# Performance work log

Measured on AMD Instinct MI355X. Metric: run time of the kernel, lower is better.

## Reference

```python
import jax, jax.numpy as jnp
import numpy as np

NU, NI, D, H, E, NQ = 200000, 100000, 64, 64, 1000000, 100000


def setup_inputs() -> dict:
    key = jax.random.key(0)
    ks = jax.random.split(key, 16)
    s = 0.05
    inp = {
        'user_emb': jax.random.normal(ks[0], (NU, D), jnp.float32) * s,
        'item_emb': jax.random.normal(ks[1], (NI, D), jnp.float32) * s,
        'W1': jax.random.normal(ks[2], (6, D, H), jnp.float32) * s,
        'b1': jnp.zeros((6, H), jnp.float32),
        'W2': jax.random.normal(ks[3], (6, H, H), jnp.float32) * s,
        'b2': jnp.zeros((6, H), jnp.float32),
        'dec_w1': jax.random.normal(ks[4], (2 * H, H), jnp.float32) * s,
        'dec_b1': jnp.zeros((H,), jnp.float32),
        'dec_w2': jax.random.normal(ks[5], (H, 4), jnp.float32) * s,
        'dec_b2': jnp.zeros((4,), jnp.float32),
    }
    for name, k in [('edge_view', ks[6]), ('edge_save', ks[7]), ('edge_buy', ks[8])]:
        src = jax.random.randint(k, (E,), 0, NU, jnp.int64 if jax.config.jax_enable_x64 else jnp.int32)
        dst = jax.random.randint(jax.random.fold_in(k, 1), (E,), 0, NI, src.dtype)
        inp[name] = jnp.stack([src, dst])  # [2, E], row0=user, row1=item
    inp['user_ids'] = jax.random.randint(ks[9], (NQ,), 0, NU, jnp.int32)
    inp['item_ids'] = jax.random.randint(ks[10], (NQ,), 0, NI, jnp.int32)
    return inp


def _gcn_conv(h_src, src, dst, n_src, n_dst, W, b):
    # GCNConv (add_self_loops=False) on a bipartite relation:
    # out[d] = sum_e 1/sqrt(deg_src[src_e]) * 1/sqrt(deg_dst[d]) * (x W)[src_e] + b
    h = h_src @ W  # [n_src, H]
    ones = jnp.ones(src.shape[0], h.dtype)
    deg_s = jax.ops.segment_sum(ones, src, num_segments=n_src)
    deg_d = jax.ops.segment_sum(ones, dst, num_segments=n_dst)
    inv_s = jnp.where(deg_s > 0, jax.lax.rsqrt(jnp.maximum(deg_s, 1.0)), 0.0)
    inv_d = jnp.where(deg_d > 0, jax.lax.rsqrt(jnp.maximum(deg_d, 1.0)), 0.0)
    norm = inv_s[src] * inv_d[dst]  # [E]
    msg = h[src] * norm[:, None]    # [E, H]  (dominant memory traffic)
    return jax.ops.segment_sum(msg, dst, num_segments=n_dst) + b


def _hetero_layer(xu, xi, edges, W, b, aggr):
    # relations 0..2: user->item (view,save,buy); 3..5: item->user (reverses)
    item_outs = jnp.stack([_gcn_conv(xu, e[0], e[1], NU, NI, W[k], b[k])
                           for k, e in enumerate(edges)])
    user_outs = jnp.stack([_gcn_conv(xi, e[1], e[0], NI, NU, W[k + 3], b[k + 3])
                           for k, e in enumerate(edges)])
    if aggr == 'max':
        return user_outs.max(0), item_outs.max(0)
    return user_outs.sum(0), item_outs.sum(0)


def reference(user_emb, item_emb, W1, b1, W2, b2, dec_w1, dec_b1, dec_w2, dec_b2,
              edge_view, edge_save, edge_buy, user_ids, item_ids):
    edges = [edge_view, edge_save, edge_buy]
    xu, xi = _hetero_layer(user_emb, item_emb, edges, W1, b1, 'max')
    xu, xi = jax.nn.relu(xu), jax.nn.relu(xi)
    xu, xi = _hetero_layer(xu, xi, edges, W2, b2, 'sum')
    edge_emb = jnp.concatenate([xu[user_ids], xi[item_ids]], axis=-1)  # [NQ, 2H]
    h = jax.nn.relu(edge_emb @ dec_w1 + dec_b1)  # dropout in eval mode = identity
    return h @ dec_w2 + dec_b2  # [NQ, 4]
```

## Files before the change

### kernel.cpp

```cpp
#include <hip/hip_runtime.h>
#include <hip/hip_fp16.h>
#include <math.h>

#define NUV 200000
#define NIV 100000
#define EV  1000000
#define NQV 100000
#define NC  (3 * NIV + 3 * NUV)
#define EV6 (6 * EV)

struct alignas(8) H4 { __half2 a, b; };

__global__ __launch_bounds__(256) void k_tohalf(const float* __restrict__ inu,
                                                const float* __restrict__ ini,
                                                __half* __restrict__ outu,
                                                __half* __restrict__ outi) {
    const int NU4 = NUV * 16;
    const int NTOT = NU4 + NIV * 16;
    int i = blockIdx.x * 256 + threadIdx.x;
    if (i < NTOT) {
        const float* in = (i < NU4) ? inu : ini;
        __half* out = (i < NU4) ? outu : outi;
        int j = (i < NU4) ? i : (i - NU4);
        float4 v = ((const float4*)in)[j];
        H4 o;
        o.a = __floats2half2_rn(v.x, v.y);
        o.b = __floats2half2_rn(v.z, v.w);
        ((H4*)out)[j] = o;
    }
}

__global__ __launch_bounds__(256) void k_count(const int* __restrict__ e0,
                                               const int* __restrict__ e1,
                                               const int* __restrict__ e2,
                                               int* __restrict__ cnt,
                                               int* __restrict__ rk_i,
                                               int* __restrict__ rk_u) {
    int k = blockIdx.y;
    const int* ed = (k == 0) ? e0 : (k == 1) ? e1 : e2;
    int e = blockIdx.x * 256 + threadIdx.x;
    if (e < EV) {
        int u = ed[e], i = ed[EV + e];
        rk_i[(size_t)k * EV + e] = atomicAdd(&cnt[k * NIV + i], 1);
        rk_u[(size_t)k * EV + e] = atomicAdd(&cnt[3 * NIV + k * NUV + u], 1);
    }
}

__global__ __launch_bounds__(256) void k_scan1(const int* __restrict__ cnt,
                                               int* __restrict__ S,
                                               int* __restrict__ bsum,
                                               float* __restrict__ invs) {
    __shared__ int tmp[256];
    int idx = blockIdx.x * 256 + threadIdx.x;
    int v = (idx < NC) ? cnt[idx] : 0;
    if (idx < NC) invs[idx] = (v > 0) ? (1.0f / sqrtf((float)v)) : 0.0f;
    tmp[threadIdx.x] = v;
    __syncthreads();
    for (int off = 1; off < 256; off <<= 1) {
        int t = (threadIdx.x >= off) ? tmp[threadIdx.x - off] : 0;
        __syncthreads();
        tmp[threadIdx.x] += t;
        __syncthreads();
    }
    if (idx < NC) S[idx] = tmp[threadIdx.x] - v;
    if (threadIdx.x == 255) bsum[blockIdx.x] = tmp[255];
}

__global__ __launch_bounds__(64) void k_scan2(int* __restrict__ bsum, int nb) {
    int lane = threadIdx.x;
    int carry = 0;
    for (int base = 0; base < nb; base += 64) {
        int i = base + lane;
        int v = (i < nb) ? bsum[i] : 0;
        int orig = v;
        #pragma unroll
        for (int off = 1; off < 64; off <<= 1) {
            int t = __shfl_up(v, off, 64);
            if (lane >= off) v += t;
        }
        if (i < nb) bsum[i] = carry + v - orig;
        carry += __shfl(v, 63, 64);
    }
}

__global__ __launch_bounds__(256) void k_scan3(int* __restrict__ S,
                                               const int* __restrict__ bsum) {
    int idx = blockIdx.x * 256 + threadIdx.x;
    if (idx < NC) S[idx] += bsum[blockIdx.x];
    if (idx == 0) S[NC] = EV6;
}

__global__ __launch_bounds__(256) void k_fill(const int* __restrict__ e0,
                                              const int* __restrict__ e1,
                                              const int* __restrict__ e2,
                                              const float* __restrict__ invs,
                                              const int* __restrict__ S,
                                              const int* __restrict__ rk_i,
                                              const int* __restrict__ rk_u,
                                              float2* __restrict__ ent) {
    int k = blockIdx.y;
    const int* ed = (k == 0) ? e0 : (k == 1) ? e1 : e2;
    int e = blockIdx.x * 256 + threadIdx.x;
    if (e < EV) {
        int u = ed[e], i = ed[EV + e];
        float nm = invs[k * NIV + i] * invs[3 * NIV + k * NUV + u];
        int p1 = S[k * NIV + i] + rk_i[(size_t)k * EV + e];
        ent[p1] = make_float2(__int_as_float(u), nm);
        int p2 = S[3 * NIV + k * NUV + u] + rk_u[(size_t)k * EV + e];
        ent[p2] = make_float2(__int_as_float(i), nm);
    }
}

template <int MODE, bool HOUT>
__global__ __launch_bounds__(256, 4) void k_agg(const __half* __restrict__ x_i,
                                                const __half* __restrict__ x_u,
                                                const float2* __restrict__ ent,
                                                const int* __restrict__ S,
                                                const float* __restrict__ Wall,
                                                const float* __restrict__ ball,
                                                void* __restrict__ out_i,
                                                void* __restrict__ out_u) {
    __shared__ float sAcc[3][16][68];
    __shared__ int nextT;

    const int NWG = NIV / 16 + NUV / 16;
    const int q = NWG / 8, r = NWG % 8;
    int xcd = blockIdx.x % 8, pos = blockIdx.x / 8;
    int wg = (xcd < r) ? (xcd * (q + 1) + pos) : (r * (q + 1) + (xcd - r) * q + pos);

    const int nb_i = NIV / 16;
    bool item_side = wg < nb_i;
    const __half* x = item_side ? x_i : x_u;
    const float* Wb = item_side ? Wall : Wall + 3 * 4096;
    const float* bb = item_side ? ball : ball + 192;
    void* outp      = item_side ? out_i : out_u;
    int n_dst       = item_side ? NIV : NUV;
    int seg_base    = item_side ? 0 : 3 * NIV;
    int d0          = (item_side ? wg : (wg - nb_i)) * 16;

    if (threadIdx.x == 0) nextT = 32;
    __syncthreads();

    int sgid = threadIdx.x >> 3;
    int ls   = threadIdx.x & 7;
    int lane = threadIdx.x & 63;

    int task = sgid;
    while (task < 48) {
        int rel = task >> 4, node = task & 15;
        int idx = seg_base + rel * n_dst + d0 + node;
        int st = S[idx], en = S[idx + 1];

        float4 a0 = make_float4(0.f, 0.f, 0.f, 0.f);
        float4 a1 = make_float4(0.f, 0.f, 0.f, 0.f);
        for (int base = st; base < en; base += 4) {
            float2 ee[4];
            #pragma unroll
            for (int j = 0; j < 4; j++) {
                float2 e = make_float2(0.0f, 0.0f);
                if (base + j < en) e = ent[base + j];
                ee[j] = e;
            }
            float4 rr[4];
            #pragma unroll
            for (int j = 0; j < 4; j++) {
                int s = __float_as_int(ee[j].x);
                rr[j] = *(const float4*)(x + (size_t)s * 64 + ls * 8);
            }
            #pragma unroll
            for (int j = 0; j < 4; j++) {
                float nm = ee[j].y;
                const __half2* h2 = (const __half2*)&rr[j];
                float2 f0 = __half22float2(h2[0]);
                float2 f1 = __half22float2(h2[1]);
                float2 f2 = __half22float2(h2[2]);
                float2 f3 = __half22float2(h2[3]);
                a0.x = fmaf(f0.x, nm, a0.x);
                a0.y = fmaf(f0.y, nm, a0.y);
                a0.z = fmaf(f1.x, nm, a0.z);
                a0.w = fmaf(f1.y, nm, a0.w);
                a1.x = fmaf(f2.x, nm, a1.x);
                a1.y = fmaf(f2.y, nm, a1.y);
                a1.z = fmaf(f3.x, nm, a1.z);
                a1.w = fmaf(f3.y, nm, a1.w);
            }
        }
        *(float4*)&sAcc[rel][node][ls * 8]     = a0;
        *(float4*)&sAcc[rel][node][ls * 8 + 4] = a1;

        int nt = 0;
        if (ls == 0) nt = atomicAdd(&nextT, 1);
        nt = __shfl(nt, lane & 56, 64);
        task = nt;
    }
    __syncthreads();

    int r2 = threadIdx.x >> 4;
    int g  = threadIdx.x & 15;
    float4 res = make_float4(0.f, 0.f, 0.f, 0.f);
    #pragma unroll
    for (int k = 0; k < 3; k++) {
        const float* Wk = Wb + (size_t)k * 4096;
        float4 y = *(const float4*)&bb[k * 64 + g * 4];
        #pragma unroll
        for (int c = 0; c < 64; c++) {
            float a = sAcc[k][r2][c];
            float4 w = *(const float4*)&Wk[c * 64 + g * 4];
            y.x = fmaf(a, w.x, y.x);
            y.y = fmaf(a, w.y, y.y);
            y.z = fmaf(a, w.z, y.z);
            y.w = fmaf(a, w.w, y.w);
        }
        if (k == 0) {
            res = y;
        } else if (MODE == 0) {
            res.x = fmaxf(res.x, y.x); res.y = fmaxf(res.y, y.y);
            res.z = fmaxf(res.z, y.z); res.w = fmaxf(res.w, y.w);
        } else {
            res.x += y.x; res.y += y.y; res.z += y.z; res.w += y.w;
        }
    }
    if (MODE == 0) {
        res.x = fmaxf(res.x, 0.f); res.y = fmaxf(res.y, 0.f);
        res.z = fmaxf(res.z, 0.f); res.w = fmaxf(res.w, 0.f);
    }
    if (HOUT) {
        H4 o;
        o.a = __floats2half2_rn(res.x, res.y);
        o.b = __floats2half2_rn(res.z, res.w);
        *(H4*)((__half*)outp + (size_t)(d0 + r2) * 64 + g * 4) = o;
    } else {
        *(float4*)((float*)outp + (size_t)(d0 + r2) * 64 + g * 4) = res;
    }
}

__global__ __launch_bounds__(256) void k_decoder(const float* __restrict__ xu,
                                                 const float* __restrict__ xi,
                                                 const int* __restrict__ uids,
                                                 const int* __restrict__ iids,
                                                 const float* __restrict__ w1,
                                                 const float* __restrict__ b1,
                                                 const float* __restrict__ w2,
                                                 const float* __restrict__ b2,
                                                 float* __restrict__ out) {
    __shared__ float sW1[128 * 64];
    __shared__ float sE[16 * 132];
    __shared__ float sH[16 * 68];
    __shared__ float sW2[64 * 4];
    {
        const float4* wsrc = (const float4*)w1;
        float4* wdst = (float4*)sW1;
        #pragma unroll
        for (int i = 0; i < 8; i++) wdst[threadIdx.x + 256 * i] = wsrc[threadIdx.x + 256 * i];
        if (threadIdx.x < 64) {
            float4 v = ((const float4*)w2)[threadIdx.x];
            ((float4*)sW2)[threadIdx.x] = v;
        }
    }
    int q0 = blockIdx.x * 16;
    {
        int q = threadIdx.x >> 4;
        int p = threadIdx.x & 15;
        int uid = uids[q0 + q];
        int iid = iids[q0 + q];
        float4 vu = *(const float4*)&xu[(size_t)uid * 64 + p * 4];
        float4 vi = *(const float4*)&xi[(size_t)iid * 64 + p * 4];
        *(float4*)&sE[q * 132 + p * 4] = vu;
        *(float4*)&sE[q * 132 + 64 + p * 4] = vi;
    }
    __syncthreads();
    {
        int r = threadIdx.x >> 4;
        int g = threadIdx.x & 15;
        float4 y = *(const float4*)&b1[g * 4];
        #pragma unroll
        for (int c = 0; c < 128; c++) {
            float a = sE[r * 132 + c];
            float4 w = *(const float4*)&sW1[c * 64 + g * 4];
            y.x = fmaf(a, w.x, y.x);
            y.y = fmaf(a, w.y, y.y);
            y.z = fmaf(a, w.z, y.z);
            y.w = fmaf(a, w.w, y.w);
        }
        y.x = fmaxf(y.x, 0.f); y.y = fmaxf(y.y, 0.f);
        y.z = fmaxf(y.z, 0.f); y.w = fmaxf(y.w, 0.f);
        *(float4*)&sH[r * 68 + g * 4] = y;
    }
    __syncthreads();
    if (threadIdx.x < 64) {
        int q = threadIdx.x >> 2;
        int oc = threadIdx.x & 3;
        float acc = b2[oc];
        #pragma unroll
        for (int c = 0; c < 64; c++)
            acc = fmaf(sH[q * 68 + c], sW2[c * 4 + oc], acc);
        out[(size_t)(q0 + q) * 4 + oc] = acc;
    }
}

extern "C" void kernel_launch(void* const* d_in, const int* in_sizes, int n_in,
                              void* d_out, int out_size, void* d_ws, size_t ws_size,
                              hipStream_t stream) {
    const float* user_emb = (const float*)d_in[0];
    const float* item_emb = (const float*)d_in[1];
    const float* W1 = (const float*)d_in[2];
    const float* b1 = (const float*)d_in[3];
    const float* W2 = (const float*)d_in[4];
    const float* b2 = (const float*)d_in[5];
    const float* dw1 = (const float*)d_in[6];
    const float* db1 = (const float*)d_in[7];
    const float* dw2 = (const float*)d_in[8];
    const float* db2 = (const float*)d_in[9];
    const int* e0 = (const int*)d_in[10];
    const int* e1 = (const int*)d_in[11];
    const int* e2 = (const int*)d_in[12];
    const int* uids = (const int*)d_in[13];
    const int* iids = (const int*)d_in[14];
    float* out = (float*)d_out;
    (void)in_sizes; (void)n_in; (void)out_size; (void)ws_size;

    char* base = (char*)d_ws;
    size_t off = 0;
    int*    cnt  = (int*)(base + off);    off += (size_t)NC * 4;
    int*    S    = (int*)(base + off);    off += (size_t)(NC + 8) * 4;
    int*    bsum = (int*)(base + off);    off += (size_t)4096 * 4;
    float*  invs = (float*)(base + off);  off += (size_t)NC * 4;
    int*    rki  = (int*)(base + off);    off += (size_t)3 * EV * 4;
    int*    rku  = (int*)(base + off);    off += (size_t)3 * EV * 4;
    float2* ent  = (float2*)(base + off); off += (size_t)EV6 * 8;
    __half* he_u = (__half*)(base + off); off += (size_t)NUV * 64 * 2;
    __half* he_i = (__half*)(base + off); off += (size_t)NIV * 64 * 2;
    __half* xu1h = (__half*)(base + off); off += (size_t)NUV * 64 * 2;
    __half* xi1h = (__half*)(base + off); off += (size_t)NIV * 64 * 2;
    float*  xu2  = (float*)(base + off);  off += (size_t)NUV * 64 * 4;
    float*  xi2  = (float*)(base + off);  off += (size_t)NIV * 64 * 4;

    const int EB  = (EV + 255) / 256;
    const int SB1 = (NC + 255) / 256;
    const int AGGB = NIV / 16 + NUV / 16;
    const int THB = ((NUV + NIV) * 16 + 255) / 256;

    k_tohalf<<<THB, 256, 0, stream>>>(user_emb, item_emb, he_u, he_i);

    hipMemsetAsync(cnt, 0, (size_t)NC * 4, stream);
    k_count<<<dim3(EB, 3), 256, 0, stream>>>(e0, e1, e2, cnt, rki, rku);
    k_scan1<<<SB1, 256, 0, stream>>>(cnt, S, bsum, invs);
    k_scan2<<<1, 64, 0, stream>>>(bsum, SB1);
    k_scan3<<<SB1, 256, 0, stream>>>(S, bsum);
    k_fill<<<dim3(EB, 3), 256, 0, stream>>>(e0, e1, e2, invs, S, rki, rku, ent);

    k_agg<0, true><<<AGGB, 256, 0, stream>>>(he_u, he_i, ent, S, W1, b1, xi1h, xu1h);
    k_agg<1, false><<<AGGB, 256, 0, stream>>>(xu1h, xi1h, ent, S, W2, b2, xi2, xu2);

    k_decoder<<<NQV / 16, 256, 0, stream>>>(xu2, xi2, uids, iids,
                                            dw1, db1, dw2, db2, out);
}
```

Before: 1.604 ms.

## Sort CSR edges by source slice and split aggregation per side

Each destination's edge list is now bucketed into slices by source-id range (8 slices for items, 4 for users), so the gather loop walks the source embeddings in a more localized order for better cache reuse. Destination degrees are derived afterwards from the slice prefix sums in a new kernel. The aggregation kernel now handles 32 nodes per block, one 8-lane subgroup per node covering all three relations, and is launched separately for the item and user sides; the dynamic task queue and XCD remapping are dropped. Layer-2 outputs are stored in half precision and the workspace reuses scratch memory, at the cost of a larger count/scan array and possible load imbalance between nodes.

```diff
diff --git a/kernel.cpp b/kernel.cpp
--- a/kernel.cpp
+++ b/kernel.cpp
@@ -8,6 +8,11 @@
 #define NQV 100000
 #define NC  (3 * NIV + 3 * NUV)
 #define EV6 (6 * EV)
+#define NSI 8
+#define NSU 4
+#define ITB (3 * NIV * NSI)
+#define TOTB (ITB + 3 * NUV * NSU)
+#define SLICE_DIV 25000
 
 struct alignas(8) H4 { __half2 a, b; };
 
@@ -41,19 +46,19 @@
     int e = blockIdx.x * 256 + threadIdx.x;
     if (e < EV) {
         int u = ed[e], i = ed[EV + e];
-        rk_i[(size_t)k * EV + e] = atomicAdd(&cnt[k * NIV + i], 1);
-        rk_u[(size_t)k * EV + e] = atomicAdd(&cnt[3 * NIV + k * NUV + u], 1);
+        int idx1 = (k * NIV + i) * NSI + u / SLICE_DIV;
+        int idx2 = ITB + (k * NUV + u) * NSU + i / SLICE_DIV;
+        rk_i[(size_t)k * EV + e] = atomicAdd(&cnt[idx1], 1);
+        rk_u[(size_t)k * EV + e] = atomicAdd(&cnt[idx2], 1);
     }
 }
 
 __global__ __launch_bounds__(256) void k_scan1(const int* __restrict__ cnt,
                                                int* __restrict__ S,
-                                               int* __restrict__ bsum,
-                                               float* __restrict__ invs) {
+                                               int* __restrict__ bsum) {
     __shared__ int tmp[256];
     int idx = blockIdx.x * 256 + threadIdx.x;
-    int v = (idx < NC) ? cnt[idx] : 0;
-    if (idx < NC) invs[idx] = (v > 0) ? (1.0f / sqrtf((float)v)) : 0.0f;
+    int v = (idx < TOTB) ? cnt[idx] : 0;
     tmp[threadIdx.x] = v;
     __syncthreads();
     for (int off = 1; off < 256; off <<= 1) {
@@ -62,7 +67,7 @@
         tmp[threadIdx.x] += t;
         __syncthreads();
     }
-    if (idx < NC) S[idx] = tmp[threadIdx.x] - v;
+    if (idx < TOTB) S[idx] = tmp[threadIdx.x] - v;
     if (threadIdx.x == 255) bsum[blockIdx.x] = tmp[255];
 }
 
@@ -86,8 +91,19 @@
 __global__ __launch_bounds__(256) void k_scan3(int* __restrict__ S,
                                                const int* __restrict__ bsum) {
     int idx = blockIdx.x * 256 + threadIdx.x;
-    if (idx < NC) S[idx] += bsum[blockIdx.x];
-    if (idx == 0) S[NC] = EV6;
+    if (idx < TOTB) S[idx] += bsum[blockIdx.x];
+    if (idx == 0) S[TOTB] = EV6;
+}
+
+__global__ __launch_bounds__(256) void k_invd(const int* __restrict__ S,
+                                              float* __restrict__ invs) {
+    int i = blockIdx.x * 256 + threadIdx.x;
+    if (i < NC) {
+        int d;
+        if (i < 3 * NIV) { int b = i * NSI; d = S[b + NSI] - S[b]; }
+        else             { int b = ITB + (i - 3 * NIV) * NSU; d = S[b + NSU] - S[b]; }
+        invs[i] = (d > 0) ? (1.0f / sqrtf((float)d)) : 0.0f;
+    }
 }
 
 __global__ __launch_bounds__(256) void k_fill(const int* __restrict__ e0,
@@ -104,138 +120,129 @@
     if (e < EV) {
         int u = ed[e], i = ed[EV + e];
         float nm = invs[k * NIV + i] * invs[3 * NIV + k * NUV + u];
-        int p1 = S[k * NIV + i] + rk_i[(size_t)k * EV + e];
+        int p1 = S[(k * NIV + i) * NSI + u / SLICE_DIV] + rk_i[(size_t)k * EV + e];
         ent[p1] = make_float2(__int_as_float(u), nm);
-        int p2 = S[3 * NIV + k * NUV + u] + rk_u[(size_t)k * EV + e];
+        int p2 = S[ITB + (k * NUV + u) * NSU + i / SLICE_DIV] + rk_u[(size_t)k * EV + e];
         ent[p2] = make_float2(__int_as_float(i), nm);
     }
 }
 
-template <int MODE, bool HOUT>
-__global__ __launch_bounds__(256, 4) void k_agg(const __half* __restrict__ x_i,
-                                                const __half* __restrict__ x_u,
-                                                const float2* __restrict__ ent,
-                                                const int* __restrict__ S,
-                                                const float* __restrict__ Wall,
-                                                const float* __restrict__ ball,
-                                                void* __restrict__ out_i,
-                                                void* __restrict__ out_u) {
-    __shared__ float sAcc[3][16][68];
-    __shared__ int nextT;
-
-    const int NWG = NIV / 16 + NUV / 16;
-    const int q = NWG / 8, r = NWG % 8;
-    int xcd = blockIdx.x % 8, pos = blockIdx.x / 8;
-    int wg = (xcd < r) ? (xcd * (q + 1) + pos) : (r * (q + 1) + (xcd - r) * q + pos);
-
-    const int nb_i = NIV / 16;
-    bool item_side = wg < nb_i;
-    const __half* x = item_side ? x_i : x_u;
-    const float* Wb = item_side ? Wall : Wall + 3 * 4096;
-    const float* bb = item_side ? ball : ball + 192;
-    void* outp      = item_side ? out_i : out_u;
-    int n_dst       = item_side ? NIV : NUV;
-    int seg_base    = item_side ? 0 : 3 * NIV;
-    int d0          = (item_side ? wg : (wg - nb_i)) * 16;
-
-    if (threadIdx.x == 0) nextT = 32;
-    __syncthreads();
+template <int MODE, int NS, bool ITEM>
+__global__ __launch_bounds__(256) void k_agg(const __half* __restrict__ x,
+                                             const float2* __restrict__ ent,
+                                             const int* __restrict__ S,
+                                             const float* __restrict__ Wall,
+                                             const float* __restrict__ ball,
+                                             __half* __restrict__ outp) {
+    __shared__ float sAcc[3][32][68];
+    const float* Wb = ITEM ? Wall : Wall + 3 * 4096;
+    const float* bb = ITEM ? ball : ball + 192;
+    const int n_per = ITEM ? NIV : NUV;
+    int d0 = blockIdx.x * 32;
 
     int sgid = threadIdx.x >> 3;
     int ls   = threadIdx.x & 7;
-    int lane = threadIdx.x & 63;
-
-    int task = sgid;
-    while (task < 48) {
-        int rel = task >> 4, node = task & 15;
-        int idx = seg_base + rel * n_dst + d0 + node;
-        int st = S[idx], en = S[idx + 1];
-
-        float4 a0 = make_float4(0.f, 0.f, 0.f, 0.f);
-        float4 a1 = make_float4(0.f, 0.f, 0.f, 0.f);
-        for (int base = st; base < en; base += 4) {
-            float2 ee[4];
-            #pragma unroll
-            for (int j = 0; j < 4; j++) {
-                float2 e = make_float2(0.0f, 0.0f);
-                if (base + j < en) e = ent[base + j];
-                ee[j] = e;
-            }
-            float4 rr[4];
-            #pragma unroll
-            for (int j = 0; j < 4; j++) {
-                int s = __float_as_int(ee[j].x);
-                rr[j] = *(const float4*)(x + (size_t)s * 64 + ls * 8);
-            }
-            #pragma unroll
-            for (int j = 0; j < 4; j++) {
-                float nm = ee[j].y;
-                const __half2* h2 = (const __half2*)&rr[j];
-                float2 f0 = __half22float2(h2[0]);
-                float2 f1 = __half22float2(h2[1]);
-                float2 f2 = __half22float2(h2[2]);
-                float2 f3 = __half22float2(h2[3]);
-                a0.x = fmaf(f0.x, nm, a0.x);
-                a0.y = fmaf(f0.y, nm, a0.y);
-                a0.z = fmaf(f1.x, nm, a0.z);
-                a0.w = fmaf(f1.y, nm, a0.w);
-                a1.x = fmaf(f2.x, nm, a1.x);
-                a1.y = fmaf(f2.y, nm, a1.y);
-                a1.z = fmaf(f3.x, nm, a1.z);
-                a1.w = fmaf(f3.y, nm, a1.w);
-            }
-        }
-        *(float4*)&sAcc[rel][node][ls * 8]     = a0;
-        *(float4*)&sAcc[rel][node][ls * 8 + 4] = a1;
-
-        int nt = 0;
-        if (ls == 0) nt = atomicAdd(&nextT, 1);
-        nt = __shfl(nt, lane & 56, 64);
-        task = nt;
-    }
-    __syncthreads();
-
-    int r2 = threadIdx.x >> 4;
-    int g  = threadIdx.x & 15;
-    float4 res = make_float4(0.f, 0.f, 0.f, 0.f);
+    int gi   = d0 + sgid;
+
+    int sb[3][NS + 1];
     #pragma unroll
     for (int k = 0; k < 3; k++) {
-        const float* Wk = Wb + (size_t)k * 4096;
-        float4 y = *(const float4*)&bb[k * 64 + g * 4];
-        #pragma unroll
-        for (int c = 0; c < 64; c++) {
-            float a = sAcc[k][r2][c];
-            float4 w = *(const float4*)&Wk[c * 64 + g * 4];
-            y.x = fmaf(a, w.x, y.x);
-            y.y = fmaf(a, w.y, y.y);
-            y.z = fmaf(a, w.z, y.z);
-            y.w = fmaf(a, w.w, y.w);
-        }
-        if (k == 0) {
-            res = y;
-        } else if (MODE == 0) {
-            res.x = fmaxf(res.x, y.x); res.y = fmaxf(res.y, y.y);
-            res.z = fmaxf(res.z, y.z); res.w = fmaxf(res.w, y.w);
-        } else {
-            res.x += y.x; res.y += y.y; res.z += y.z; res.w += y.w;
-        }
-    }
-    if (MODE == 0) {
-        res.x = fmaxf(res.x, 0.f); res.y = fmaxf(res.y, 0.f);
-        res.z = fmaxf(res.z, 0.f); res.w = fmaxf(res.w, 0.f);
-    }
-    if (HOUT) {
+        int b = ITEM ? (k * NIV + gi) * NS : (ITB + (k * n_per + gi) * NS);
+        #pragma unroll
+        for (int j = 0; j <= NS; j++) sb[k][j] = S[b + j];
+    }
+
+    float a[3][8];
+    #pragma unroll
+    for (int k = 0; k < 3; k++)
+        #pragma unroll
+        for (int j = 0; j < 8; j++) a[k][j] = 0.f;
+
+    for (int p = 0; p < NS; p++) {
+        #pragma unroll
+        for (int k = 0; k < 3; k++) {
+            int st = sb[k][p], en = sb[k][p + 1];
+            for (int base = st; base < en; base += 4) {
+                float2 ee[4];
+                #pragma unroll
+                for (int j = 0; j < 4; j++) {
+                    float2 e = make_float2(0.0f, 0.0f);
+                    if (base + j < en) e = ent[base + j];
+                    ee[j] = e;
+                }
+                float4 rr[4];
+                #pragma unroll
+                for (int j = 0; j < 4; j++) {
+                    int s = __float_as_int(ee[j].x);
+                    rr[j] = *(const float4*)(x + (size_t)s * 64 + ls * 8);
+                }
+                #pragma unroll
+                for (int j = 0; j < 4; j++) {
+                    float nm = ee[j].y;
+                    const __half2* h2 = (const __half2*)&rr[j];
+                    float2 f0 = __half22float2(h2[0]);
+                    float2 f1 = __half22float2(h2[1]);
+                    float2 f2 = __half22float2(h2[2]);
+                    float2 f3 = __half22float2(h2[3]);
+                    a[k][0] = fmaf(f0.x, nm, a[k][0]);
+                    a[k][1] = fmaf(f0.y, nm, a[k][1]);
+                    a[k][2] = fmaf(f1.x, nm, a[k][2]);
+                    a[k][3] = fmaf(f1.y, nm, a[k][3]);
+                    a[k][4] = fmaf(f2.x, nm, a[k][4]);
+                    a[k][5] = fmaf(f2.y, nm, a[k][5]);
+                    a[k][6] = fmaf(f3.x, nm, a[k][6]);
+                    a[k][7] = fmaf(f3.y, nm, a[k][7]);
+                }
+            }
+        }
+    }
+    #pragma unroll
+    for (int k = 0; k < 3; k++) {
+        *(float4*)&sAcc[k][sgid][ls * 8]     = make_float4(a[k][0], a[k][1], a[k][2], a[k][3]);
+        *(float4*)&sAcc[k][sgid][ls * 8 + 4] = make_float4(a[k][4], a[k][5], a[k][6], a[k][7]);
+    }
+    __syncthreads();
+
+    int g = threadIdx.x & 15;
+    #pragma unroll
+    for (int half = 0; half < 2; half++) {
+        int r = half * 16 + (threadIdx.x >> 4);
+        float4 res = make_float4(0.f, 0.f, 0.f, 0.f);
+        #pragma unroll
+        for (int k = 0; k < 3; k++) {
+            const float* Wk = Wb + (size_t)k * 4096;
+            float4 y = *(const float4*)&bb[k * 64 + g * 4];
+            #pragma unroll
+            for (int c = 0; c < 64; c++) {
+                float av = sAcc[k][r][c];
+                float4 w = *(const float4*)&Wk[c * 64 + g * 4];
+                y.x = fmaf(av, w.x, y.x);
+                y.y = fmaf(av, w.y, y.y);
+                y.z = fmaf(av, w.z, y.z);
+                y.w = fmaf(av, w.w, y.w);
+            }
+            if (k == 0) {
+                res = y;
+            } else if (MODE == 0) {
+                res.x = fmaxf(res.x, y.x); res.y = fmaxf(res.y, y.y);
+                res.z = fmaxf(res.z, y.z); res.w = fmaxf(res.w, y.w);
+            } else {
+                res.x += y.x; res.y += y.y; res.z += y.z; res.w += y.w;
+            }
+        }
+        if (MODE == 0) {
+            res.x = fmaxf(res.x, 0.f); res.y = fmaxf(res.y, 0.f);
+            res.z = fmaxf(res.z, 0.f); res.w = fmaxf(res.w, 0.f);
+        }
         H4 o;
         o.a = __floats2half2_rn(res.x, res.y);
         o.b = __floats2half2_rn(res.z, res.w);
-        *(H4*)((__half*)outp + (size_t)(d0 + r2) * 64 + g * 4) = o;
-    } else {
-        *(float4*)((float*)outp + (size_t)(d0 + r2) * 64 + g * 4) = res;
-    }
-}
-
-__global__ __launch_bounds__(256) void k_decoder(const float* __restrict__ xu,
-                                                 const float* __restrict__ xi,
+        *(H4*)(outp + (size_t)(d0 + r) * 64 + g * 4) = o;
+    }
+}
+
+__global__ __launch_bounds__(256) void k_decoder(const __half* __restrict__ xu,
+                                                 const __half* __restrict__ xi,
                                                  const int* __restrict__ uids,
                                                  const int* __restrict__ iids,
                                                  const float* __restrict__ w1,
@@ -263,10 +270,12 @@
         int p = threadIdx.x & 15;
         int uid = uids[q0 + q];
         int iid = iids[q0 + q];
-        float4 vu = *(const float4*)&xu[(size_t)uid * 64 + p * 4];
-        float4 vi = *(const float4*)&xi[(size_t)iid * 64 + p * 4];
-        *(float4*)&sE[q * 132 + p * 4] = vu;
-        *(float4*)&sE[q * 132 + 64 + p * 4] = vi;
+        H4 vu = *(const H4*)(xu + (size_t)uid * 64 + p * 4);
+        H4 vi = *(const H4*)(xi + (size_t)iid * 64 + p * 4);
+        float2 u0 = __half22float2(vu.a), u1 = __half22float2(vu.b);
+        float2 i0 = __half22float2(vi.a), i1 = __half22float2(vi.b);
+        *(float4*)&sE[q * 132 + p * 4] = make_float4(u0.x, u0.y, u1.x, u1.y);
+        *(float4*)&sE[q * 132 + 64 + p * 4] = make_float4(i0.x, i0.y, i1.x, i1.y);
     }
     __syncthreads();
     {
@@ -321,37 +330,41 @@
 
     char* base = (char*)d_ws;
     size_t off = 0;
-    int*    cnt  = (int*)(base + off);    off += (size_t)NC * 4;
-    int*    S    = (int*)(base + off);    off += (size_t)(NC + 8) * 4;
-    int*    bsum = (int*)(base + off);    off += (size_t)4096 * 4;
+    int*    S    = (int*)(base + off);    off += (size_t)(TOTB + 16) * 4;
+    int*    bsum = (int*)(base + off);    off += (size_t)20480 * 4;
     float*  invs = (float*)(base + off);  off += (size_t)NC * 4;
-    int*    rki  = (int*)(base + off);    off += (size_t)3 * EV * 4;
-    int*    rku  = (int*)(base + off);    off += (size_t)3 * EV * 4;
     float2* ent  = (float2*)(base + off); off += (size_t)EV6 * 8;
     __half* he_u = (__half*)(base + off); off += (size_t)NUV * 64 * 2;
     __half* he_i = (__half*)(base + off); off += (size_t)NIV * 64 * 2;
     __half* xu1h = (__half*)(base + off); off += (size_t)NUV * 64 * 2;
     __half* xi1h = (__half*)(base + off); off += (size_t)NIV * 64 * 2;
-    float*  xu2  = (float*)(base + off);  off += (size_t)NUV * 64 * 4;
-    float*  xi2  = (float*)(base + off);  off += (size_t)NIV * 64 * 4;
+    char* scr = base + off;
+    int*    cnt  = (int*)scr;
+    int*    rki  = (int*)(scr + (size_t)TOTB * 4);
+    int*    rku  = rki + (size_t)3 * EV;
+    __half* xu2h = (__half*)scr;
+    __half* xi2h = xu2h + (size_t)NUV * 64;
 
     const int EB  = (EV + 255) / 256;
-    const int SB1 = (NC + 255) / 256;
-    const int AGGB = NIV / 16 + NUV / 16;
+    const int SCB = TOTB / 256;
+    const int NCB = (NC + 255) / 256;
     const int THB = ((NUV + NIV) * 16 + 255) / 256;
 
     k_tohalf<<<THB, 256, 0, stream>>>(user_emb, item_emb, he_u, he_i);
 
-    hipMemsetAsync(cnt, 0, (size_t)NC * 4, stream);
+    hipMemsetAsync(cnt, 0, (size_t)TOTB * 4, stream);
     k_count<<<dim3(EB, 3), 256, 0, stream>>>(e0, e1, e2, cnt, rki, rku);
-    k_scan1<<<SB1, 256, 0, stream>>>(cnt, S, bsum, invs);
-    k_scan2<<<1, 64, 0, stream>>>(bsum, SB1);
-    k_scan3<<<SB1, 256, 0, stream>>>(S, bsum);
+    k_scan1<<<SCB, 256, 0, stream>>>(cnt, S, bsum);
+    k_scan2<<<1, 64, 0, stream>>>(bsum, SCB);
+    k_scan3<<<SCB, 256, 0, stream>>>(S, bsum);
+    k_invd<<<NCB, 256, 0, stream>>>(S, invs);
     k_fill<<<dim3(EB, 3), 256, 0, stream>>>(e0, e1, e2, invs, S, rki, rku, ent);
 
-    k_agg<0, true><<<AGGB, 256, 0, stream>>>(he_u, he_i, ent, S, W1, b1, xi1h, xu1h);
-    k_agg<1, false><<<AGGB, 256, 0, stream>>>(xu1h, xi1h, ent, S, W2, b2, xi2, xu2);
-
-    k_decoder<<<NQV / 16, 256, 0, stream>>>(xu2, xi2, uids, iids,
+    k_agg<0, NSI, true ><<<NIV / 32, 256, 0, stream>>>(he_u, ent, S, W1, b1, xi1h);
+    k_agg<0, NSU, false><<<NUV / 32, 256, 0, stream>>>(he_i, ent, S, W1, b1, xu1h);
+    k_agg<1, NSI, true ><<<NIV / 32, 256, 0, stream>>>(xu1h, ent, S, W2, b2, xi2h);
+    k_agg<1, NSU, false><<<NUV / 32, 256, 0, stream>>>(xi1h, ent, S, W2, b2, xu2h);
+
+    k_decoder<<<NQV / 16, 256, 0, stream>>>(xu2h, xi2h, uids, iids,
                                             dw1, db1, dw2, db2, out);
 }
```

New measurement: 3.469 ms. 2.16x slower.
